# Optimization experiments

Measured on AMD Instinct MI355X. Metric: run time of the kernel, lower is better.

## Reference

```python
import jax, jax.numpy as jnp
import numpy as np

B, S, D = 4, 2048, 1024
H = 16
HD = D // H  # 64


def setup_inputs() -> dict:
    key = jax.random.key(0)
    ks = jax.random.split(key, 9)
    sc = 1.0 / np.sqrt(D)
    return {
        "hidden_states": jax.random.normal(ks[0], (B, S, D), jnp.float32),
        "Wq": jax.random.normal(ks[1], (D, D), jnp.float32) * sc,
        "bq": jnp.zeros((D,), jnp.float32),
        "Wk": jax.random.normal(ks[2], (D, D), jnp.float32) * sc,
        "bk": jnp.zeros((D,), jnp.float32),
        "Wv": jax.random.normal(ks[3], (D, D), jnp.float32) * sc,
        "bv": jnp.zeros((D,), jnp.float32),
        "Wo": jax.random.normal(ks[4], (D, D), jnp.float32) * sc,
        "bo": jnp.zeros((D,), jnp.float32),
    }


def _rope_emb(seq_len, head_dim, dtype):
    # Faithful to torch buffer: emb = cat(sin(pos*inv_freq), cos(pos*inv_freq))
    inv_freq = 1.0 / (10000.0 ** (jnp.arange(0, head_dim, 2, dtype=jnp.float32) / head_dim))
    sinusoid = jnp.arange(seq_len, dtype=jnp.float32)[:, None] * inv_freq[None, :]  # [S, hd/2]
    return jnp.concatenate([jnp.sin(sinusoid), jnp.cos(sinusoid)], axis=-1).astype(dtype)  # [S, hd]


def _rotate(x, c, s):
    # x: [B,H,S,hd]; c,s: [1,1,S,hd/2]
    x1, x2 = x[..., : HD // 2], x[..., HD // 2 :]
    return jnp.concatenate([x1 * c - x2 * s, x2 * c + x1 * s], axis=-1)


def reference(hidden_states, Wq, bq, Wk, bk, Wv, bv, Wo, bo):
    b, s, d = hidden_states.shape

    def proj(W, bias):
        y = jnp.einsum("bsd,ed->bse", hidden_states, W) + bias
        return y.reshape(b, s, H, HD).transpose(0, 2, 1, 3)  # [B,H,S,hd]

    q, k, v = proj(Wq, bq), proj(Wk, bk), proj(Wv, bv)

    emb = _rope_emb(s, HD, hidden_states.dtype)
    # NOTE: original code names first half 'cos' though the buffer stores sin first.
    c = emb[None, None, :, : HD // 2]
    sn = emb[None, None, :, HD // 2 :]
    q = _rotate(q, c, sn)
    k = _rotate(k, c, sn)

    scores = jnp.einsum("bhqd,bhkd->bhqk", q, k) / jnp.sqrt(jnp.asarray(HD, hidden_states.dtype))
    probs = jax.nn.softmax(scores, axis=-1)
    ctx = jnp.einsum("bhqk,bhkd->bhqd", probs, v)
    ctx = ctx.transpose(0, 2, 1, 3).reshape(b, s, d)  # [B,S,D]
    return jnp.einsum("bsd,ed->bse", ctx, Wo) + bo
```

## Files before the change

### kernel.cpp

```cpp
#include <hip/hip_runtime.h>
#include <cmath>

#define B_ 4
#define S_ 2048
#define D_ 1024
#define H_ 16
#define HD_ 64

typedef __attribute__((ext_vector_type(8))) _Float16 half8;
typedef __attribute__((ext_vector_type(2))) _Float16 half2t;
typedef __attribute__((ext_vector_type(2))) __fp16 fp16x2;
typedef __attribute__((ext_vector_type(4))) float floatx4;
typedef __attribute__((ext_vector_type(16))) float floatx16;

union H2U { unsigned u; half2t h; fp16x2 f; };
__device__ __forceinline__ unsigned hpack2(float a, float b) {
    H2U x; x.h[0] = (_Float16)a; x.h[1] = (_Float16)b; return x.u;
}
__device__ __forceinline__ unsigned pkrtz(float a, float b) {
    H2U x; x.f = __builtin_amdgcn_cvt_pkrtz(a, b); return x.u;
}
__device__ __forceinline__ float h_lo(unsigned u) { H2U x; x.u = u; return (float)x.h[0]; }
__device__ __forceinline__ float h_hi(unsigned u) { H2U x; x.u = u; return (float)x.h[1]; }

__global__ __launch_bounds__(256)
void conv_x(const float* __restrict__ x, unsigned short* __restrict__ o, int n)
{
    const int i = (blockIdx.x * 256 + threadIdx.x) * 8;
    if (i >= n) return;
    const float4 a = *(const float4*)(x + i);
    const float4 b = *(const float4*)(x + i + 4);
    *(uint4*)(o + i) = make_uint4(hpack2(a.x, a.y), hpack2(a.z, a.w),
                                  hpack2(b.x, b.y), hpack2(b.z, b.w));
}

__global__ __launch_bounds__(256)
void conv_weights(const float* __restrict__ Wq, const float* __restrict__ Wk,
                  const float* __restrict__ Wv, const float* __restrict__ Wo,
                  const float* __restrict__ bq, const float* __restrict__ bk,
                  const float* __restrict__ bv,
                  unsigned short* __restrict__ Wqkvf, unsigned short* __restrict__ Wof,
                  float* __restrict__ bqkv)
{
    const int bxx = blockIdx.x;
    const int t = threadIdx.x;
    if (bxx < 2048) {
        const int w = bxx >> 9;
        const int i = ((bxx & 511) * 256 + t) * 8;
        const float* src = (w == 0) ? Wq : (w == 1) ? Wk : (w == 2) ? Wv : Wo;
        const float4 a = *(const float4*)(src + i);
        const float4 b = *(const float4*)(src + i + 4);
        const uint4 v = make_uint4(hpack2(a.x, a.y), hpack2(a.z, a.w),
                                   hpack2(b.x, b.y), hpack2(b.z, b.w));
        if (w < 3)
            *(uint4*)(Wqkvf + (size_t)w * 1048576 + i) = v;
        else
            *(uint4*)(Wof + i) = v;
    } else {
        const int idx = t * 4;
        *(float4*)(bqkv + idx)        = *(const float4*)(bq + idx);
        *(float4*)(bqkv + 1024 + idx) = *(const float4*)(bk + idx);
        *(float4*)(bqkv + 2048 + idx) = *(const float4*)(bv + idx);
    }
}

template<int OBF>
__global__ __launch_bounds__(256, 2)
void gemm_half(const unsigned short* __restrict__ Ap, const unsigned short* __restrict__ Bp,
               const float* __restrict__ bias, void* __restrict__ Cout,
               int M, int N, int K)
{
    __shared__ uint4 ASH[512];
    __shared__ uint4 BSH[512];

    const int tid = threadIdx.x;
    const int bm = blockIdx.x * 128;
    const int bn = blockIdx.y * 128;
    const int w = tid >> 6, l = tid & 63;
    const int wm = (w & 1) * 64, wn = (w >> 1) * 64;

    floatx4 acc[4][4];
#pragma unroll
    for (int i = 0; i < 4; ++i)
#pragma unroll
        for (int j = 0; j < 4; ++j)
#pragma unroll
            for (int r = 0; r < 4; ++r) acc[i][j][r] = 0.f;

    const int r0 = tid >> 1, scb = (tid & 1) * 2;
    const size_t ga = (size_t)(bm + r0) * K + scb * 8;
    const size_t gb = (size_t)(bn + r0) * K + scb * 8;
    const int f0 = ((r0 >> 4) << 6) + (scb << 4) + (r0 & 15);

    const half8* pA = (const half8*)ASH;
    const half8* pB = (const half8*)BSH;
    const int am = (wm >> 4) * 64 + l;
    const int bnf = (wn >> 4) * 64 + l;

    uint4 vA0 = *(const uint4*)(Ap + ga);
    uint4 vA1 = *(const uint4*)(Ap + ga + 8);
    uint4 vB0 = *(const uint4*)(Bp + gb);
    uint4 vB1 = *(const uint4*)(Bp + gb + 8);

    for (int k0 = 0; k0 < K; k0 += 32) {
        __syncthreads();
        ASH[f0] = vA0; ASH[f0 + 16] = vA1;
        BSH[f0] = vB0; BSH[f0 + 16] = vB1;
        __syncthreads();

        const int kn = (k0 + 32 < K) ? k0 + 32 : k0;
        vA0 = *(const uint4*)(Ap + ga + kn);
        vA1 = *(const uint4*)(Ap + ga + kn + 8);
        vB0 = *(const uint4*)(Bp + gb + kn);
        vB1 = *(const uint4*)(Bp + gb + kn + 8);

        half8 a[4];
#pragma unroll
        for (int i = 0; i < 4; ++i) a[i] = pA[am + i * 64];
#pragma unroll
        for (int j = 0; j < 4; ++j) {
            const half8 b = pB[bnf + j * 64];
#pragma unroll
            for (int i = 0; i < 4; ++i)
                acc[i][j] = __builtin_amdgcn_mfma_f32_16x16x32_f16(a[i], b, acc[i][j], 0, 0, 0);
        }
    }

    const int cr = (l >> 4) << 2;
    const int cc = l & 15;
#pragma unroll
    for (int j = 0; j < 4; ++j) {
        const int col = bn + wn + j * 16 + cc;
        const float bv = bias[col];
#pragma unroll
        for (int i = 0; i < 4; ++i) {
            const int row = bm + wm + i * 16 + cr;
#pragma unroll
            for (int r = 0; r < 4; ++r) {
                const float vv = acc[i][j][r] + bv;
                if (OBF) {
                    ((unsigned short*)Cout)[(size_t)(row + r) * N + col] =
                        (unsigned short)(hpack2(vv, vv) & 0xffffu);
                } else {
                    ((float*)Cout)[(size_t)(row + r) * N + col] = vv;
                }
            }
        }
    }
}

__global__ __launch_bounds__(256)
void prep_fused(const unsigned short* __restrict__ qkv,
                unsigned short* __restrict__ Qf, unsigned short* __restrict__ Kfo,
                unsigned short* __restrict__ Vt)
{
    __shared__ unsigned T[64][65];
    const int bx = blockIdx.x;
    const int t = threadIdx.x;
    if (bx < B_ * S_) {
        const int s = bx & (S_ - 1);
        const size_t rbase = (size_t)bx * 3072;
        const size_t obase = (size_t)bx * D_;
        const int h = t >> 4;
        const int i2 = (t & 15) * 2;
        const float kfreq = 0.28782313662425572f;
        const float KS = 0.18033688011112042f;

        const float f0 = expf(-(float)i2 * kfreq);
        const float f1 = expf(-(float)(i2 + 1) * kfreq);
        const float t0 = (float)s * f0, t1 = (float)s * f1;
        const float sn0 = sinf(t0), cs0 = cosf(t0);
        const float sn1 = sinf(t1), cs1 = cosf(t1);

        const size_t c1 = (size_t)h * 64 + i2;
        const size_t c2 = c1 + 32;

        const unsigned uq1 = *(const unsigned*)(qkv + rbase + c1);
        const unsigned uq2 = *(const unsigned*)(qkv + rbase + c2);
        const unsigned uk1 = *(const unsigned*)(qkv + rbase + 1024 + c1);
        const unsigned uk2 = *(const unsigned*)(qkv + rbase + 1024 + c2);
        const float q1x = h_lo(uq1), q1y = h_hi(uq1);
        const float q2x = h_lo(uq2), q2y = h_hi(uq2);
        const float k1x = h_lo(uk1), k1y = h_hi(uk1);
        const float k2x = h_lo(uk2), k2y = h_hi(uk2);

        *(unsigned*)(Qf + obase + c1) = hpack2(q1x * sn0 - q2x * cs0, q1y * sn1 - q2y * cs1);
        *(unsigned*)(Qf + obase + c2) = hpack2(q2x * sn0 + q1x * cs0, q2y * sn1 + q1y * cs1);
        *(unsigned*)(Kfo + obase + c1) = hpack2((k1x * sn0 - k2x * cs0) * KS, (k1y * sn1 - k2y * cs1) * KS);
        *(unsigned*)(Kfo + obase + c2) = hpack2((k2x * sn0 + k1x * cs0) * KS, (k2y * sn1 + k1y * cs1) * KS);
    } else {
        const int vb = bx - B_ * S_;
        const int st = vb & 31;
        const int h  = (vb >> 5) & 15;
        const int b  = vb >> 9;
        const int s0 = st * 64;
#pragma unroll
        for (int it = 0; it < 2; ++it) {
            const int idx = it * 256 + t;
            const int row = idx >> 3;
            const int c8 = (idx & 7) * 8;
            const uint4 u = *(const uint4*)(qkv + ((size_t)(b * S_ + s0 + row)) * 3072 + 2048 + h * 64 + c8);
            T[row][c8+0] = u.x & 0xffffu; T[row][c8+1] = u.x >> 16;
            T[row][c8+2] = u.y & 0xffffu; T[row][c8+3] = u.y >> 16;
            T[row][c8+4] = u.z & 0xffffu; T[row][c8+5] = u.z >> 16;
            T[row][c8+6] = u.w & 0xffffu; T[row][c8+7] = u.w >> 16;
        }
        __syncthreads();
        const int d = t >> 2;
        const int scg = (t & 3) * 16;
        unsigned u[8];
#pragma unroll
        for (int ii = 0; ii < 8; ++ii)
            u[ii] = T[scg + 2*ii][d] | (T[scg + 2*ii + 1][d] << 16);
        unsigned short* dst = Vt + ((size_t)((b * H_ + h) * 64 + d)) * S_ + s0 + scg;
        *(uint4*)(dst)     = make_uint4(u[0], u[1], u[2], u[3]);
        *(uint4*)(dst + 8) = make_uint4(u[4], u[5], u[6], u[7]);
    }
}

__global__ __launch_bounds__(256)
void attn_mfma32(const unsigned short* __restrict__ Qf,
                 const unsigned short* __restrict__ Kfi,
                 const unsigned short* __restrict__ Vt,
                 unsigned short* __restrict__ Cf)
{
    __shared__ uint4 KF[512];
    __shared__ uint4 VF[512];

    const int t = threadIdx.x;
    const int i = blockIdx.x;
    const int xcd = i & 7, j = i >> 3;
    const int bh = xcd * 8 + (j >> 4);
    const int qblk = j & 15;
    const int b = bh >> 4, h = bh & 15;

    const int w = t >> 6, l = t & 63;
    const int lq = l & 31, h5 = l >> 5;
    const int qrow = qblk * 128 + w * 32 + lq;

    half8 qf[4];
    const unsigned short* qp = Qf + ((size_t)(b * S_ + qrow)) * D_ + h * 64 + h5 * 8;
#pragma unroll
    for (int kc = 0; kc < 4; ++kc) qf[kc] = *(const half8*)(qp + kc * 16);

    floatx16 o0, o1, o2, z16;
#pragma unroll
    for (int r = 0; r < 16; ++r) { o0[r] = 0.f; o1[r] = 0.f; o2[r] = 0.f; z16[r] = 0.f; }

    union { unsigned u[4]; half8 s; } onesf;
    const unsigned ov = (lq == 0) ? 0x3C003C00u : 0u;
    onesf.u[0] = ov; onesf.u[1] = ov; onesf.u[2] = ov; onesf.u[3] = ov;

    const int sr = t >> 2, sc = t & 3;
    const unsigned short* gK0 = Kfi + ((size_t)(b * S_ + sr)) * D_ + h * 64 + sc * 16;
    const unsigned short* gV0 = Vt + ((size_t)((b * H_ + h) * 64 + sr)) * S_ + sc * 16;
    const int e0 = (sr >> 5) * 256 + sc * 64 + (sr & 31);

    const half8* pK = (const half8*)KF;
    const half8* pV = (const half8*)VF;

    uint4 ka  = *(const uint4*)(gK0);
    uint4 kb2 = *(const uint4*)(gK0 + 8);
    uint4 va  = *(const uint4*)(gV0);
    uint4 vb2 = *(const uint4*)(gV0 + 8);

    for (int kt = 0; kt < 32; ++kt) {
        __syncthreads();
        KF[e0] = ka; KF[e0 + 32] = kb2;
        VF[e0] = va; VF[e0 + 32] = vb2;
        __syncthreads();

        const int kn = (kt < 31) ? kt + 1 : kt;
        const unsigned short* gK = gK0 + (size_t)kn * 64 * D_;
        const unsigned short* gV = gV0 + (size_t)kn * 64;
        ka  = *(const uint4*)(gK);
        kb2 = *(const uint4*)(gK + 8);
        va  = *(const uint4*)(gV);
        vb2 = *(const uint4*)(gV + 8);

        floatx16 st0 = __builtin_amdgcn_mfma_f32_32x32x16_f16(pK[l],          qf[0], z16, 0, 0, 0);
        floatx16 st1 = __builtin_amdgcn_mfma_f32_32x32x16_f16(pK[4 * 64 + l], qf[0], z16, 0, 0, 0);
#pragma unroll
        for (int kc = 1; kc < 4; ++kc) {
            st0 = __builtin_amdgcn_mfma_f32_32x32x16_f16(pK[kc * 64 + l],       qf[kc], st0, 0, 0, 0);
            st1 = __builtin_amdgcn_mfma_f32_32x32x16_f16(pK[(4 + kc) * 64 + l], qf[kc], st1, 0, 0, 0);
        }

        unsigned pu0[8], pu1[8];
#pragma unroll
        for (int g = 0; g < 8; ++g) {
            pu0[g] = pkrtz(__builtin_amdgcn_exp2f(st0[2 * g]),
                           __builtin_amdgcn_exp2f(st0[2 * g + 1]));
            pu1[g] = pkrtz(__builtin_amdgcn_exp2f(st1[2 * g]),
                           __builtin_amdgcn_exp2f(st1[2 * g + 1]));
        }

#pragma unroll
        for (int kc = 0; kc < 4; ++kc) {
            const unsigned* pus = (kc >> 1) ? pu1 : pu0;
            const int g0 = (kc & 1) * 4;
            const unsigned own0 = h5 ? pus[g0 + 2] : pus[g0 + 0];
            const unsigned srv0 = h5 ? pus[g0 + 0] : pus[g0 + 2];
            const unsigned own1 = h5 ? pus[g0 + 3] : pus[g0 + 1];
            const unsigned srv1 = h5 ? pus[g0 + 1] : pus[g0 + 3];
            const unsigned par0 = (unsigned)__shfl_xor((int)srv0, 32, 64);
            const unsigned par1 = (unsigned)__shfl_xor((int)srv1, 32, 64);
            union { unsigned u[4]; half8 s; } pf;
            pf.u[0] = h5 ? par0 : own0;
            pf.u[1] = h5 ? par1 : own1;
            pf.u[2] = h5 ? own0 : par0;
            pf.u[3] = h5 ? own1 : par1;
            o0 = __builtin_amdgcn_mfma_f32_32x32x16_f16(pV[kc * 64 + l],       pf.s, o0, 0, 0, 0);
            o1 = __builtin_amdgcn_mfma_f32_32x32x16_f16(pV[(4 + kc) * 64 + l], pf.s, o1, 0, 0, 0);
            o2 = __builtin_amdgcn_mfma_f32_32x32x16_f16(onesf.s,               pf.s, o2, 0, 0, 0);
        }
    }

    const float lpart = o2[0];
    const float lothr = __shfl_xor(lpart, 32, 64);
    const float lsum = h5 ? lothr : lpart;
    const float inv = 1.0f / lsum;

    const size_t cbase = ((size_t)(b * S_ + qrow)) * D_ + h * 64;
#pragma unroll
    for (int rq = 0; rq < 4; ++rq) {
        const int d0 = rq * 8 + h5 * 4;
        const uint2 y0 = make_uint2(hpack2(o0[4*rq+0] * inv, o0[4*rq+1] * inv),
                                    hpack2(o0[4*rq+2] * inv, o0[4*rq+3] * inv));
        const uint2 y1 = make_uint2(hpack2(o1[4*rq+0] * inv, o1[4*rq+1] * inv),
                                    hpack2(o1[4*rq+2] * inv, o1[4*rq+3] * inv));
        *(uint2*)(Cf + cbase + d0)      = y0;
        *(uint2*)(Cf + cbase + 32 + d0) = y1;
    }
}

extern "C" void kernel_launch(void* const* d_in, const int* in_sizes, int n_in,
                              void* d_out, int out_size, void* d_ws, size_t ws_size,
                              hipStream_t stream) {
    (void)in_sizes; (void)n_in; (void)out_size; (void)ws_size;
    const float* X  = (const float*)d_in[0];
    const float* Wq = (const float*)d_in[1];
    const float* bq = (const float*)d_in[2];
    const float* Wk = (const float*)d_in[3];
    const float* bk = (const float*)d_in[4];
    const float* Wv = (const float*)d_in[5];
    const float* bv = (const float*)d_in[6];
    const float* Wo = (const float*)d_in[7];
    const float* bo = (const float*)d_in[8];
    float* out = (float*)d_out;

    char* ws = (char*)d_ws;
#define OFF(mb) (ws + ((size_t)(mb) << 20))
    unsigned short* Xf    = (unsigned short*)OFF(0);
    unsigned short* qkv16 = (unsigned short*)OFF(16);
    unsigned short* Qf    = (unsigned short*)OFF(64);
    unsigned short* Kfb   = (unsigned short*)OFF(80);
    unsigned short* Vtb   = (unsigned short*)OFF(96);
    unsigned short* Wqkvf = (unsigned short*)OFF(112);
    unsigned short* Wof   = (unsigned short*)OFF(118);
    float*          bqkv  = (float*)OFF(120);
    unsigned short* Cf    = (unsigned short*)OFF(0);
#undef OFF

    const int NX = B_ * S_ * D_;
    conv_x<<<NX / 2048, 256, 0, stream>>>(X, Xf, NX);
    conv_weights<<<2049, 256, 0, stream>>>(Wq, Wk, Wv, Wo, bq, bk, bv,
                                           Wqkvf, Wof, bqkv);
    gemm_half<1><<<dim3(64, 24), 256, 0, stream>>>(Xf, Wqkvf, bqkv,
                                                   qkv16, B_*S_, 3 * D_, D_);
    prep_fused<<<B_*S_ + 2048, 256, 0, stream>>>(qkv16, Qf, Kfb, Vtb);
    attn_mfma32<<<1024, 256, 0, stream>>>(Qf, Kfb, Vtb, Cf);
    gemm_half<0><<<dim3(64, 8), 256, 0, stream>>>(Cf, Wof, bo, out, B_*S_, D_, D_);
}
```

Measured before the change: 336.2 us.

## Double-buffer K/V LDS tiles and use permlane32_swap for P exchange

Converts the attention kernel's single-buffered K/V shared memory into a double buffer with one barrier per iteration, prefetching two tiles ahead so LDS stores of the next tile overlap with MFMA work on the current one. It replaces the ds_bpermute-based cross-half shuffles with permlane32_swap to exchange P fragments and the final row sum between lane halves. It also adds s_setprio around MFMA blocks to favor matrix issue. Shared memory use doubles, which may lower occupancy, and the hand-written waitcnt/barrier asm depends on correct ordering.

```diff
diff --git a/kernel.cpp b/kernel.cpp
--- a/kernel.cpp
+++ b/kernel.cpp
@@ -12,6 +12,7 @@
 typedef __attribute__((ext_vector_type(2))) __fp16 fp16x2;
 typedef __attribute__((ext_vector_type(4))) float floatx4;
 typedef __attribute__((ext_vector_type(16))) float floatx16;
+typedef __attribute__((ext_vector_type(2))) unsigned uint2v;
 
 union H2U { unsigned u; half2t h; fp16x2 f; };
 __device__ __forceinline__ unsigned hpack2(float a, float b) {
@@ -22,6 +23,10 @@
 }
 __device__ __forceinline__ float h_lo(unsigned u) { H2U x; x.u = u; return (float)x.h[0]; }
 __device__ __forceinline__ float h_hi(unsigned u) { H2U x; x.u = u; return (float)x.h[1]; }
+
+__device__ __forceinline__ void barrier_lgkm() {
+    asm volatile("s_waitcnt lgkmcnt(0)\n\ts_barrier" ::: "memory");
+}
 
 __global__ __launch_bounds__(256)
 void conv_x(const float* __restrict__ x, unsigned short* __restrict__ o, int n)
@@ -224,8 +229,8 @@
                  const unsigned short* __restrict__ Vt,
                  unsigned short* __restrict__ Cf)
 {
-    __shared__ uint4 KF[512];
-    __shared__ uint4 VF[512];
+    __shared__ uint4 KF[2][512];
+    __shared__ uint4 VF[2][512];
 
     const int t = threadIdx.x;
     const int i = blockIdx.x;
@@ -256,28 +261,44 @@
     const unsigned short* gV0 = Vt + ((size_t)((b * H_ + h) * 64 + sr)) * S_ + sc * 16;
     const int e0 = (sr >> 5) * 256 + sc * 64 + (sr & 31);
 
-    const half8* pK = (const half8*)KF;
-    const half8* pV = (const half8*)VF;
-
     uint4 ka  = *(const uint4*)(gK0);
     uint4 kb2 = *(const uint4*)(gK0 + 8);
     uint4 va  = *(const uint4*)(gV0);
     uint4 vb2 = *(const uint4*)(gV0 + 8);
-
-    for (int kt = 0; kt < 32; ++kt) {
-        __syncthreads();
-        KF[e0] = ka; KF[e0 + 32] = kb2;
-        VF[e0] = va; VF[e0 + 32] = vb2;
-        __syncthreads();
-
-        const int kn = (kt < 31) ? kt + 1 : kt;
-        const unsigned short* gK = gK0 + (size_t)kn * 64 * D_;
-        const unsigned short* gV = gV0 + (size_t)kn * 64;
+    KF[0][e0] = ka; KF[0][e0 + 32] = kb2;
+    VF[0][e0] = va; VF[0][e0 + 32] = vb2;
+    {
+        const unsigned short* gK = gK0 + (size_t)64 * D_;
+        const unsigned short* gV = gV0 + 64;
         ka  = *(const uint4*)(gK);
         kb2 = *(const uint4*)(gK + 8);
         va  = *(const uint4*)(gV);
         vb2 = *(const uint4*)(gV + 8);
-
+    }
+    __syncthreads();
+
+    for (int kt = 0; kt < 32; ++kt) {
+        const int cur = kt & 1;
+
+        if (kt < 31) {
+            uint4* wK = KF[cur ^ 1];
+            uint4* wV = VF[cur ^ 1];
+            wK[e0] = ka; wK[e0 + 32] = kb2;
+            wV[e0] = va; wV[e0 + 32] = vb2;
+        }
+        if (kt < 30) {
+            const unsigned short* gK = gK0 + (size_t)(kt + 2) * 64 * D_;
+            const unsigned short* gV = gV0 + (size_t)(kt + 2) * 64;
+            ka  = *(const uint4*)(gK);
+            kb2 = *(const uint4*)(gK + 8);
+            va  = *(const uint4*)(gV);
+            vb2 = *(const uint4*)(gV + 8);
+        }
+
+        const half8* pK = (const half8*)KF[cur];
+        const half8* pV = (const half8*)VF[cur];
+
+        __builtin_amdgcn_s_setprio(1);
         floatx16 st0 = __builtin_amdgcn_mfma_f32_32x32x16_f16(pK[l],          qf[0], z16, 0, 0, 0);
         floatx16 st1 = __builtin_amdgcn_mfma_f32_32x32x16_f16(pK[4 * 64 + l], qf[0], z16, 0, 0, 0);
 #pragma unroll
@@ -285,6 +306,7 @@
             st0 = __builtin_amdgcn_mfma_f32_32x32x16_f16(pK[kc * 64 + l],       qf[kc], st0, 0, 0, 0);
             st1 = __builtin_amdgcn_mfma_f32_32x32x16_f16(pK[(4 + kc) * 64 + l], qf[kc], st1, 0, 0, 0);
         }
+        __builtin_amdgcn_s_setprio(0);
 
         unsigned pu0[8], pu1[8];
 #pragma unroll
@@ -295,31 +317,31 @@
                            __builtin_amdgcn_exp2f(st1[2 * g + 1]));
         }
 
+        __builtin_amdgcn_s_setprio(1);
 #pragma unroll
         for (int kc = 0; kc < 4; ++kc) {
             const unsigned* pus = (kc >> 1) ? pu1 : pu0;
             const int g0 = (kc & 1) * 4;
-            const unsigned own0 = h5 ? pus[g0 + 2] : pus[g0 + 0];
-            const unsigned srv0 = h5 ? pus[g0 + 0] : pus[g0 + 2];
-            const unsigned own1 = h5 ? pus[g0 + 3] : pus[g0 + 1];
-            const unsigned srv1 = h5 ? pus[g0 + 1] : pus[g0 + 3];
-            const unsigned par0 = (unsigned)__shfl_xor((int)srv0, 32, 64);
-            const unsigned par1 = (unsigned)__shfl_xor((int)srv1, 32, 64);
+            const uint2v r02 = __builtin_amdgcn_permlane32_swap(pus[g0 + 0], pus[g0 + 2], false, false);
+            const uint2v r13 = __builtin_amdgcn_permlane32_swap(pus[g0 + 1], pus[g0 + 3], false, false);
             union { unsigned u[4]; half8 s; } pf;
-            pf.u[0] = h5 ? par0 : own0;
-            pf.u[1] = h5 ? par1 : own1;
-            pf.u[2] = h5 ? own0 : par0;
-            pf.u[3] = h5 ? own1 : par1;
+            pf.u[0] = r02[0];
+            pf.u[1] = r13[0];
+            pf.u[2] = r02[1];
+            pf.u[3] = r13[1];
             o0 = __builtin_amdgcn_mfma_f32_32x32x16_f16(pV[kc * 64 + l],       pf.s, o0, 0, 0, 0);
             o1 = __builtin_amdgcn_mfma_f32_32x32x16_f16(pV[(4 + kc) * 64 + l], pf.s, o1, 0, 0, 0);
             o2 = __builtin_amdgcn_mfma_f32_32x32x16_f16(onesf.s,               pf.s, o2, 0, 0, 0);
         }
-    }
-
-    const float lpart = o2[0];
-    const float lothr = __shfl_xor(lpart, 32, 64);
-    const float lsum = h5 ? lothr : lpart;
-    const float inv = 1.0f / lsum;
+        __builtin_amdgcn_s_setprio(0);
+
+        if (kt < 31) barrier_lgkm();
+    }
+
+    union { float f; unsigned u; } lc; lc.f = o2[0];
+    const uint2v lr = __builtin_amdgcn_permlane32_swap(lc.u, lc.u, false, false);
+    union { unsigned u; float f; } ls; ls.u = lr[0];
+    const float inv = 1.0f / ls.f;
 
     const size_t cbase = ((size_t)(b * S_ + qrow)) * D_ + h * 64;
 #pragma unroll
```

Measured after the change: 311.2 us. -7.4%, faster.
